# Performance work log

Hardware: AMD Instinct MI355X
Metric: run time of the kernel (lower is better)

The kernel has to match this reference:

```python
import jax, jax.numpy as jnp
import numpy as np

T = 4          # number of atom types (H, C, N, O)
D = 384        # aev_length
H0, H1, H2 = 160, 128, 96
B, A = 2048, 64
ALPHA = 0.1    # CELU alpha


def celu(x, alpha=ALPHA):
    return jnp.where(x > 0, x, alpha * jnp.expm1(x / alpha))


def setup_inputs() -> dict:
    key = jax.random.key(0)
    ks = jax.random.split(key, 6)
    species = jax.random.randint(ks[0], (B, A), 0, T, dtype=jnp.int32)
    aev = jax.random.normal(ks[1], (B, A, D), dtype=jnp.float32)

    def w(k, shape, fan_in):
        return (jax.random.normal(k, shape, dtype=jnp.float32) / np.sqrt(fan_in)).astype(jnp.float32)

    # stacked per-type weights: leading axis T
    W0 = w(ks[2], (T, D, H0), D);   b0 = jnp.zeros((T, H0), jnp.float32)
    W1 = w(ks[3], (T, H0, H1), H0); b1 = jnp.zeros((T, H1), jnp.float32)
    W2 = w(ks[4], (T, H1, H2), H1); b2 = jnp.zeros((T, H2), jnp.float32)
    W3 = w(ks[5], (T, H2, 1), H2);  b3 = jnp.zeros((T, 1), jnp.float32)
    return dict(species=species, aev=aev,
                W0=W0, b0=b0, W1=W1, b1=b1, W2=W2, b2=b2, W3=W3, b3=b3)


def reference(species, aev, W0, b0, W1, b1, W2, b2, W3, b3):
    # species: [B, A] int32 in [0, T); aev: [B, A, D]
    sp = species.reshape(-1)            # [N]
    x = aev.reshape(-1, D)              # [N, D]
    # Run every type's MLP over all atoms (T is small), then select per atom.
    h = celu(jnp.einsum('nd,tdh->tnh', x, W0) + b0[:, None, :])   # [T, N, H0]
    h = celu(jnp.einsum('tnh,thk->tnk', h, W1) + b1[:, None, :])  # [T, N, H1]
    h = celu(jnp.einsum('tnk,tkm->tnm', h, W2) + b2[:, None, :])  # [T, N, H2]
    o = jnp.einsum('tnm,tmo->tno', h, W3) + b3[:, None, :]        # [T, N, 1]
    o = o[..., 0]                                                  # [T, N]
    per_atom = jnp.take_along_axis(o, sp[None, :], axis=0)[0]     # [N]
    energies = per_atom.reshape(species.shape).sum(axis=1)        # [B]
    return species, energies
```

## Files before the change

### kernel.cpp

```cpp
#include <hip/hip_runtime.h>
#include <hip/hip_bf16.h>

#define DD 384
#define NB 2048
#define NA 64
#define NN (NB*NA)

using bhalf8 = __attribute__((ext_vector_type(8))) __bf16;
using f32x4  = __attribute__((ext_vector_type(4))) float;
typedef unsigned short u16;
typedef unsigned char u8;

#define AS1 __attribute__((address_space(1)))
#define AS3 __attribute__((address_space(3)))

__device__ __forceinline__ void gl_lds16(const void* g, void* l) {
  __builtin_amdgcn_global_load_lds((const AS1 void*)g, (AS3 void*)l, 16, 0, 0);
}

__device__ __forceinline__ u16 f2b(float f) {
  __hip_bfloat16 h = __float2bfloat16(f);
  union { __hip_bfloat16 h; u16 u; } c; c.h = h; return c.u;
}
__device__ __forceinline__ float b2f(u16 u) {
  union { unsigned int i; float f; } c; c.i = ((unsigned int)u) << 16; return c.f;
}
__device__ __forceinline__ float celu_f(float v) {
  return v > 0.f ? v : 0.1f * (__expf(v * 10.f) - 1.f);
}
__device__ __forceinline__ bhalf8 pack8(float4 a, float4 b) {
  union { u16 us[8]; bhalf8 v; } t;
  t.us[0]=f2b(a.x); t.us[1]=f2b(a.y); t.us[2]=f2b(a.z); t.us[3]=f2b(a.w);
  t.us[4]=f2b(b.x); t.us[5]=f2b(b.y); t.us[6]=f2b(b.z); t.us[7]=f2b(b.w);
  return t.v;
}


__global__ void k_prep(const int* __restrict__ species, int* __restrict__ cursors,
                       float* __restrict__ out_sp, int* __restrict__ sorted,
                       const float* __restrict__ W0, const float* __restrict__ W1,
                       const float* __restrict__ W2, const float* __restrict__ W3,
                       u16* __restrict__ W0img, u16* __restrict__ W1img,
                       u16* __restrict__ W2img, u16* __restrict__ W3B) {
  int tid = threadIdx.x;
  int id = blockIdx.x * 256 + tid;
  if (blockIdx.x < 512) {
    __shared__ int lcnt[4];
    __shared__ int lbase[4];
    if (tid < 4) lcnt[tid] = 0;
    __syncthreads();
    int s = species[id];
    out_sp[id] = (float)s;
    int lpos = atomicAdd(&lcnt[s], 1);
    __syncthreads();
    if (tid < 4) lbase[tid] = atomicAdd(&cursors[tid], lcnt[tid]);
    __syncthreads();
    sorted[s * NN + lbase[s] + lpos] = id;
  }
  if (id < 245760) {
    int t = id / 61440, r1 = id % 61440;
    int kc = r1 / 5120, r2 = r1 % 5120;
    int r = r2 >> 5, rem = r2 & 31, s = rem >> 3, e = rem & 7;
    int k = kc * 32 + (s ^ ((r >> 1) & 3)) * 8 + e;
    W0img[id] = f2b(W0[t * 61440 + k * 160 + r]);
  } else if ((id -= 245760) < 81920) {
    int t = id / 20480, r1 = id % 20480;
    int kc = r1 / 4096, r2 = r1 % 4096;
    int r = r2 >> 5, rem = r2 & 31, s = rem >> 3, e = rem & 7;
    int k = kc * 32 + (s ^ ((r >> 1) & 3)) * 8 + e;
    W1img[id] = f2b(W1[t * 20480 + k * 128 + r]);
  } else if ((id -= 81920) < 65536) {
    int t = id / 16384, r1 = id % 16384;
    int kc = r1 / 4096, r2 = r1 % 4096;
    int r = r2 >> 5, rem = r2 & 31, s = rem >> 3, e = rem & 7;
    u16 v = 0;
    if (r < 96) {
      int k = kc * 32 + (s ^ ((r >> 1) & 3)) * 8 + e;
      v = f2b(W2[t * 12288 + k * 96 + r]);
    }
    W2img[id] = v;
  } else if ((id -= 65536) < 384) {
    W3B[id] = f2b(W3[id]);
  }
}


__global__ __launch_bounds__(256, 5) void k_mlp(
    const float* __restrict__ aev, const int* __restrict__ sorted,
    const int* __restrict__ counts,
    const u16* __restrict__ W0img, const u16* __restrict__ W1img,
    const u16* __restrict__ W2img, const u16* __restrict__ W3B,
    const float* __restrict__ b0, const float* __restrict__ b1,
    const float* __restrict__ b2, const float* __restrict__ b3,
    float* __restrict__ atom_out)
{
  int type = blockIdx.x, tile = blockIdx.y;
  int cnt = counts[type];
  if (tile * 64 >= cnt) return;

  __shared__ uint4 smem4[1536];
  u8* smem = (u8*)smem4;
  u8*  Ast = smem;
  u16* sH0 = (u16*)smem;
  u16* sH1 = (u16*)smem;
  u16* sH2 = (u16*)smem;

  int tid = threadIdx.x, lane = tid & 63, w = tid >> 6;
  int wm = w & 1, wn = w >> 1, l15 = lane & 15, lk = lane >> 4;
  int base = type * NN + tile * 64, nvalid = min(64, cnt - tile * 64);

  int arow0 = w * 16 + (lane >> 3), arow1 = arow0 + 8;
  const float* a0 = aev + (size_t)sorted[base + min(arow0, nvalid - 1)] * DD
                    + (((lane & 7) ^ (arow0 & 7)) << 2);
  const float* a1 = aev + (size_t)sorted[base + min(arow1, nvalid - 1)] * DD
                    + (((lane & 7) ^ (arow1 & 7)) << 2);
  u8* dA = Ast + w * 2048;

#define STG_A(KC, B_) do { \
    gl_lds16(a0 + (KC) * 32, dA + (B_) * 8192); \
    gl_lds16(a1 + (KC) * 32, dA + (B_) * 8192 + 1024); \
  } while (0)

  int bsw = (lk ^ ((l15 >> 1) & 3)) << 4;
  const u8* gB0 = (const u8*)W0img + (size_t)type * 122880 + ((wn * 80 + l15) << 6) + bsw;
  int aoff0 = (wm * 32 + l15) * 128, aoff1 = aoff0 + 2048;
  int sAa = (((2 * lk)     ^ (l15 & 7)) << 4);
  int sAb = (((2 * lk + 1) ^ (l15 & 7)) << 4);

#define TOPW(WN) do { \
  asm volatile("s_waitcnt vmcnt(" #WN ")" ::: "memory"); \
  __builtin_amdgcn_sched_barrier(0); \
  __builtin_amdgcn_s_barrier(); \
  __builtin_amdgcn_sched_barrier(0); } while (0)
#define TAILW() do { \
  asm volatile("s_waitcnt lgkmcnt(0)" ::: "memory"); \
  __builtin_amdgcn_sched_barrier(0); \
  __builtin_amdgcn_s_barrier(); \
  __builtin_amdgcn_sched_barrier(0); } while (0)

  f32x4 acc0[2][5];
  #pragma unroll
  for (int mt = 0; mt < 2; ++mt)
    #pragma unroll
    for (int nt = 0; nt < 5; ++nt) acc0[mt][nt] = f32x4{0.f, 0.f, 0.f, 0.f};

  bhalf8 bf[5];
  STG_A(0, 0);
  #pragma unroll
  for (int nt = 0; nt < 5; ++nt) bf[nt] = *(const bhalf8*)(gB0 + nt * 1024);
  STG_A(1, 1);

#define PHA(KC, WN) \
  TOPW(WN); \
  { const u8* bA = Ast + ((KC) % 3) * 8192; \
    bhalf8 af0 = pack8(*(const float4*)(bA + aoff0 + sAa), *(const float4*)(bA + aoff0 + sAb)); \
    bhalf8 af1 = pack8(*(const float4*)(bA + aoff1 + sAa), *(const float4*)(bA + aoff1 + sAb)); \
    _Pragma("unroll") \
    for (int nt = 0; nt < 5; ++nt) { \
      acc0[0][nt] = __builtin_amdgcn_mfma_f32_16x16x32_bf16(af0, bf[nt], acc0[0][nt], 0, 0, 0); \
      acc0[1][nt] = __builtin_amdgcn_mfma_f32_16x16x32_bf16(af1, bf[nt], acc0[1][nt], 0, 0, 0); \
    } \
    if ((KC) < 11) { \
      _Pragma("unroll") \
      for (int nt = 0; nt < 5; ++nt) \
        bf[nt] = *(const bhalf8*)(gB0 + ((KC) + 1) * 10240 + nt * 1024); \
    } } \
  if ((KC) < 10) STG_A((KC) + 2, ((KC) + 2) % 3);

  PHA(0, 2)  PHA(1, 2)  PHA(2, 2)  PHA(3, 2)  PHA(4, 2)  PHA(5, 2)
  PHA(6, 2)  PHA(7, 2)  PHA(8, 2)  PHA(9, 2)  PHA(10, 2) PHA(11, 0)
#undef PHA
#undef STG_A

  TAILW();

  #pragma unroll
  for (int mt = 0; mt < 2; ++mt)
    #pragma unroll
    for (int nt = 0; nt < 5; ++nt) {
      int col = wn * 80 + nt * 16 + l15;
      float bias = b0[type * 160 + col];
      #pragma unroll
      for (int i = 0; i < 4; ++i) {
        int row = wm * 32 + mt * 16 + lk * 4 + i;
        sH0[row * 168 + col] = f2b(celu_f(acc0[mt][nt][i] + bias));
      }
    }
  TAILW();

  const u8* gW1 = (const u8*)W1img + (size_t)type * 40960 + ((wn * 64 + l15) << 6) + bsw;
  f32x4 acc1[2][4];
  #pragma unroll
  for (int mt = 0; mt < 2; ++mt)
    #pragma unroll
    for (int nt = 0; nt < 4; ++nt) acc1[mt][nt] = f32x4{0.f, 0.f, 0.f, 0.f};

  #pragma unroll
  for (int kc = 0; kc < 5; ++kc) {
    bhalf8 af0 = *(const bhalf8*)&sH0[(wm * 32 + l15) * 168 + kc * 32 + lk * 8];
    bhalf8 af1 = *(const bhalf8*)&sH0[(wm * 32 + 16 + l15) * 168 + kc * 32 + lk * 8];
    bhalf8 bw[4];
    #pragma unroll
    for (int nt = 0; nt < 4; ++nt)
      bw[nt] = *(const bhalf8*)(gW1 + kc * 8192 + nt * 1024);
    #pragma unroll
    for (int nt = 0; nt < 4; ++nt) {
      acc1[0][nt] = __builtin_amdgcn_mfma_f32_16x16x32_bf16(af0, bw[nt], acc1[0][nt], 0, 0, 0);
      acc1[1][nt] = __builtin_amdgcn_mfma_f32_16x16x32_bf16(af1, bw[nt], acc1[1][nt], 0, 0, 0);
    }
  }
  TAILW();

  #pragma unroll
  for (int mt = 0; mt < 2; ++mt)
    #pragma unroll
    for (int nt = 0; nt < 4; ++nt) {
      int col = wn * 64 + nt * 16 + l15;
      float bias = b1[type * 128 + col];
      #pragma unroll
      for (int i = 0; i < 4; ++i) {
        int row = wm * 32 + mt * 16 + lk * 4 + i;
        sH1[row * 136 + col] = f2b(celu_f(acc1[mt][nt][i] + bias));
      }
    }
  TAILW();

  const u8* gW2 = (const u8*)W2img + (size_t)type * 32768 + ((wn * 48 + l15) << 6) + bsw;
  f32x4 acc2[2][3];
  #pragma unroll
  for (int mt = 0; mt < 2; ++mt)
    #pragma unroll
    for (int nt = 0; nt < 3; ++nt) acc2[mt][nt] = f32x4{0.f, 0.f, 0.f, 0.f};

  #pragma unroll
  for (int kc = 0; kc < 4; ++kc) {
    bhalf8 af0 = *(const bhalf8*)&sH1[(wm * 32 + l15) * 136 + kc * 32 + lk * 8];
    bhalf8 af1 = *(const bhalf8*)&sH1[(wm * 32 + 16 + l15) * 136 + kc * 32 + lk * 8];
    bhalf8 bw[3];
    #pragma unroll
    for (int nt = 0; nt < 3; ++nt)
      bw[nt] = *(const bhalf8*)(gW2 + kc * 8192 + nt * 1024);
    #pragma unroll
    for (int nt = 0; nt < 3; ++nt) {
      acc2[0][nt] = __builtin_amdgcn_mfma_f32_16x16x32_bf16(af0, bw[nt], acc2[0][nt], 0, 0, 0);
      acc2[1][nt] = __builtin_amdgcn_mfma_f32_16x16x32_bf16(af1, bw[nt], acc2[1][nt], 0, 0, 0);
    }
  }
  TAILW();

  #pragma unroll
  for (int mt = 0; mt < 2; ++mt)
    #pragma unroll
    for (int nt = 0; nt < 3; ++nt) {
      int col = wn * 48 + nt * 16 + l15;
      float bias = b2[type * 96 + col];
      #pragma unroll
      for (int i = 0; i < 4; ++i) {
        int row = wm * 32 + mt * 16 + lk * 4 + i;
        sH2[row * 104 + col] = f2b(celu_f(acc2[mt][nt][i] + bias));
      }
    }
  TAILW();

  {
    int atom = tid >> 2;
    int q = tid & 3;
    const u16* w3 = W3B + type * 96 + q * 24;
    const u16* hrow = sH2 + atom * 104 + q * 24;
    float s = 0.f;
    #pragma unroll
    for (int i = 0; i < 3; ++i) {
      union { bhalf8 v; u16 u[8]; } hu, wu2;
      hu.v = *(const bhalf8*)&hrow[i * 8];
      wu2.v = *(const bhalf8*)&w3[i * 8];
      #pragma unroll
      for (int j = 0; j < 8; ++j)
        s += b2f(hu.u[j]) * b2f(wu2.u[j]);
    }
    s += __shfl_xor(s, 1);
    s += __shfl_xor(s, 2);
    if (q == 0 && atom < nvalid)
      atom_out[sorted[base + atom]] = s + b3[type];
  }
}

__global__ void k_reduce(const float* __restrict__ atom_out, float* __restrict__ out_e) {
  int mol = blockIdx.x;
  int lane = threadIdx.x;
  float v = atom_out[mol * 64 + lane];
  #pragma unroll
  for (int m = 32; m >= 1; m >>= 1) v += __shfl_xor(v, m);
  if (lane == 0) out_e[mol] = v;
}


extern "C" void kernel_launch(void* const* d_in, const int* in_sizes, int n_in,
                              void* d_out, int out_size, void* d_ws, size_t ws_size,
                              hipStream_t stream) {
  const int*   species = (const int*)d_in[0];
  const float* aev = (const float*)d_in[1];
  const float* W0 = (const float*)d_in[2];
  const float* b0 = (const float*)d_in[3];
  const float* W1 = (const float*)d_in[4];
  const float* b1 = (const float*)d_in[5];
  const float* W2 = (const float*)d_in[6];
  const float* b2 = (const float*)d_in[7];
  const float* W3 = (const float*)d_in[8];
  const float* b3 = (const float*)d_in[9];
  float* out = (float*)d_out;

  unsigned char* ws = (unsigned char*)d_ws;
  int* cursors = (int*)(ws + 0);
  int* sorted = (int*)(ws + 64);
  float* atom_out = (float*)(ws + 2097216);
  u16* W0img = (u16*)(ws + 2621504);
  u16* W1img = (u16*)(ws + 3113024);
  u16* W2img = (u16*)(ws + 3276864);
  u16* W3B   = (u16*)(ws + 3407936);

  hipMemsetAsync(cursors, 0, 16, stream);
  k_prep<<<1538, 256, 0, stream>>>(species, cursors, out, sorted,
        W0, W1, W2, W3, W0img, W1img, W2img, W3B);
  k_mlp<<<dim3(4, 2048), 256, 0, stream>>>(aev, sorted, cursors,
        W0img, W1img, W2img, W3B, b0, b1, b2, b3, atom_out);
  k_reduce<<<NB, 64, 0, stream>>>(atom_out, out + NN);
}
```

Before: 72.80 us.

## Deepen A prefetch to 4 stages, compact grid, fuse energy reduction via atomics

Three changes at once. The aev staging ring grows from 3 to 4 LDS buffers, so three K-chunks are in flight, and the per-phase wait counts are retuned. The 2D grid of 4x2048 blocks, most of which exit immediately, becomes a 1D grid of 2051 blocks that maps directly onto the occupied tiles of each type using the counts. The separate per-molecule reduce kernel is removed: k_prep zeroes the energies and each atom's output is atomically added into its molecule's energy, which saves a launch and the atom_out buffer but adds atomic contention and makes the summation order nondeterministic.

```diff
diff --git a/kernel.cpp b/kernel.cpp
--- a/kernel.cpp
+++ b/kernel.cpp
@@ -37,7 +37,7 @@
 
 
 __global__ void k_prep(const int* __restrict__ species, int* __restrict__ cursors,
-                       float* __restrict__ out_sp, int* __restrict__ sorted,
+                       float* __restrict__ out, int* __restrict__ sorted,
                        const float* __restrict__ W0, const float* __restrict__ W1,
                        const float* __restrict__ W2, const float* __restrict__ W3,
                        u16* __restrict__ W0img, u16* __restrict__ W1img,
@@ -50,12 +50,14 @@
     if (tid < 4) lcnt[tid] = 0;
     __syncthreads();
     int s = species[id];
-    out_sp[id] = (float)s;
+    out[id] = (float)s;
     int lpos = atomicAdd(&lcnt[s], 1);
     __syncthreads();
     if (tid < 4) lbase[tid] = atomicAdd(&cursors[tid], lcnt[tid]);
     __syncthreads();
     sorted[s * NN + lbase[s] + lpos] = id;
+  } else if (blockIdx.x < 520) {
+    out[NN + (blockIdx.x - 512) * 256 + tid] = 0.f;
   }
   if (id < 245760) {
     int t = id / 61440, r1 = id % 61440;
@@ -92,13 +94,19 @@
     const u16* __restrict__ W2img, const u16* __restrict__ W3B,
     const float* __restrict__ b0, const float* __restrict__ b1,
     const float* __restrict__ b2, const float* __restrict__ b3,
-    float* __restrict__ atom_out)
+    float* __restrict__ outE)
 {
-  int type = blockIdx.x, tile = blockIdx.y;
-  int cnt = counts[type];
+  int c0 = counts[0], c1 = counts[1], c2 = counts[2], c3 = counts[3];
+  int T0 = (c0 + 63) >> 6, T1 = (c1 + 63) >> 6, T2 = (c2 + 63) >> 6;
+  int b = blockIdx.x, type, tile;
+  if (b < T0)              { type = 0; tile = b; }
+  else if ((b -= T0) < T1) { type = 1; tile = b; }
+  else if ((b -= T1) < T2) { type = 2; tile = b; }
+  else { type = 3; tile = b - T2; }
+  int cnt = (type == 0) ? c0 : (type == 1) ? c1 : (type == 2) ? c2 : c3;
   if (tile * 64 >= cnt) return;
 
-  __shared__ uint4 smem4[1536];
+  __shared__ uint4 smem4[2048];
   u8* smem = (u8*)smem4;
   u8*  Ast = smem;
   u16* sH0 = (u16*)smem;
@@ -149,10 +157,11 @@
   #pragma unroll
   for (int nt = 0; nt < 5; ++nt) bf[nt] = *(const bhalf8*)(gB0 + nt * 1024);
   STG_A(1, 1);
+  STG_A(2, 2);
 
 #define PHA(KC, WN) \
   TOPW(WN); \
-  { const u8* bA = Ast + ((KC) % 3) * 8192; \
+  { const u8* bA = Ast + ((KC) % 4) * 8192; \
     bhalf8 af0 = pack8(*(const float4*)(bA + aoff0 + sAa), *(const float4*)(bA + aoff0 + sAb)); \
     bhalf8 af1 = pack8(*(const float4*)(bA + aoff1 + sAa), *(const float4*)(bA + aoff1 + sAb)); \
     _Pragma("unroll") \
@@ -165,10 +174,10 @@
       for (int nt = 0; nt < 5; ++nt) \
         bf[nt] = *(const bhalf8*)(gB0 + ((KC) + 1) * 10240 + nt * 1024); \
     } } \
-  if ((KC) < 10) STG_A((KC) + 2, ((KC) + 2) % 3);
-
-  PHA(0, 2)  PHA(1, 2)  PHA(2, 2)  PHA(3, 2)  PHA(4, 2)  PHA(5, 2)
-  PHA(6, 2)  PHA(7, 2)  PHA(8, 2)  PHA(9, 2)  PHA(10, 2) PHA(11, 0)
+  if ((KC) < 9) STG_A((KC) + 3, ((KC) + 3) % 4);
+
+  PHA(0, 4)   PHA(1, 7)   PHA(2, 14)  PHA(3, 14)  PHA(4, 14)  PHA(5, 14)
+  PHA(6, 14)  PHA(7, 14)  PHA(8, 14)  PHA(9, 14)  PHA(10, 12) PHA(11, 10)
 #undef PHA
 #undef STG_A
 
@@ -279,18 +288,11 @@
     }
     s += __shfl_xor(s, 1);
     s += __shfl_xor(s, 2);
-    if (q == 0 && atom < nvalid)
-      atom_out[sorted[base + atom]] = s + b3[type];
-  }
-}
-
-__global__ void k_reduce(const float* __restrict__ atom_out, float* __restrict__ out_e) {
-  int mol = blockIdx.x;
-  int lane = threadIdx.x;
-  float v = atom_out[mol * 64 + lane];
-  #pragma unroll
-  for (int m = 32; m >= 1; m >>= 1) v += __shfl_xor(v, m);
-  if (lane == 0) out_e[mol] = v;
+    if (q == 0 && atom < nvalid) {
+      int ai = sorted[base + atom];
+      atomicAdd(&outE[ai >> 6], s + b3[type]);
+    }
+  }
 }
 
 
@@ -312,16 +314,14 @@
   unsigned char* ws = (unsigned char*)d_ws;
   int* cursors = (int*)(ws + 0);
   int* sorted = (int*)(ws + 64);
-  float* atom_out = (float*)(ws + 2097216);
-  u16* W0img = (u16*)(ws + 2621504);
-  u16* W1img = (u16*)(ws + 3113024);
-  u16* W2img = (u16*)(ws + 3276864);
-  u16* W3B   = (u16*)(ws + 3407936);
+  u16* W0img = (u16*)(ws + 2097216);
+  u16* W1img = (u16*)(ws + 2588736);
+  u16* W2img = (u16*)(ws + 2752576);
+  u16* W3B   = (u16*)(ws + 2883648);
 
   hipMemsetAsync(cursors, 0, 16, stream);
   k_prep<<<1538, 256, 0, stream>>>(species, cursors, out, sorted,
         W0, W1, W2, W3, W0img, W1img, W2img, W3B);
-  k_mlp<<<dim3(4, 2048), 256, 0, stream>>>(aev, sorted, cursors,
-        W0img, W1img, W2img, W3B, b0, b1, b2, b3, atom_out);
-  k_reduce<<<NB, 64, 0, stream>>>(atom_out, out + NN);
-}
+  k_mlp<<<2051, 256, 0, stream>>>(aev, sorted, cursors,
+        W0img, W1img, W2img, W3B, b0, b1, b2, b3, out + NN);
+}
```

Result: slower. 84.65 us (+16.3%).
